# Optimization experiments

Hardware: AMD Instinct MI355X
Metric: run time of the kernel (lower is better)

The kernel has to match this reference:

```python
import jax, jax.numpy as jnp
import numpy as np

SCALE = 56  # output spatial resolution, HW = 3136
K = 3       # n_neighbors for top-k softmin scoring


def avg_pool3(x):
    # F.avg_pool2d(x, 3, 1, 1) with count_include_pad=True -> zero-padded sum / 9
    s = jax.lax.reduce_window(x, 0.0, jax.lax.add, (1, 1, 3, 3), (1, 1, 1, 1),
                              ((0, 0), (0, 0), (1, 1), (1, 1)))
    return s / 9.0


def resize_to(x, hw):
    # F.interpolate(mode='bilinear', align_corners=False) == jax.image half-pixel bilinear
    B, C, _, _ = x.shape
    return jax.image.resize(x, (B, C, hw, hw), method='bilinear')


def add_coords(x):
    # CoordConv AddCoords: append normalized x/y coordinate channels in [-1, 1]
    B, C, H, W = x.shape
    xx = jnp.broadcast_to(jnp.linspace(-1.0, 1.0, W, dtype=x.dtype)[None, :], (H, W))
    yy = jnp.broadcast_to(jnp.linspace(-1.0, 1.0, H, dtype=x.dtype)[:, None], (H, W))
    xxb = jnp.broadcast_to(xx[None, None], (B, 1, H, W))
    yyb = jnp.broadcast_to(yy[None, None], (B, 1, H, W))
    return jnp.concatenate([x, xxb, yyb], axis=1)


def setup_inputs() -> dict:
    key = jax.random.key(0)
    k1, k2, k3, k4, k5 = jax.random.split(key, 5)
    p1 = jax.random.normal(k1, (8, 256, 56, 56), dtype=jnp.float32)
    p2 = jax.random.normal(k2, (8, 512, 28, 28), dtype=jnp.float32)
    p3 = jax.random.normal(k3, (8, 1024, 14, 14), dtype=jnp.float32)
    W = jax.random.normal(k4, (1792, 1794), dtype=jnp.float32) * 0.02  # 1x1 CoordConv weight
    b = jnp.zeros((1792,), dtype=jnp.float32)
    C = jax.random.normal(k5, (1792, 3136), dtype=jnp.float32) * 0.05  # centroid bank
    return {"p1": p1, "p2": p2, "p3": p3, "W": W, "b": b, "C": C}


def reference(p1, p2, p3, W, b, C):
    # Descriptor: smooth each pyramid level, upsample to 56x56, concat -> (B,1792,56,56)
    o1 = avg_pool3(p1)
    o2 = resize_to(avg_pool3(p2), SCALE)
    o3 = resize_to(avg_pool3(p3), SCALE)
    sample = jnp.concatenate([o1, o2, o3], axis=1)
    # CoordConv 1x1
    xc = add_coords(sample)  # (B, 1794, 56, 56)
    phi = jnp.einsum('bchw,oc->bohw', xc, W) + b[None, :, None, None]
    B = phi.shape[0]
    phi_p = phi.reshape(B, 1792, SCALE * SCALE).transpose(0, 2, 1)  # (B, HW, C)
    # pairwise squared distances via expansion + matmul: (B, HW, 3136)
    features = jnp.sum(phi_p * phi_p, axis=2, keepdims=True)
    centers = jnp.sum(C * C, axis=0, keepdims=True)
    dist = features + centers - 2.0 * jnp.matmul(phi_p, C)
    dist = jnp.sqrt(jnp.maximum(dist, 0.0))
    # top-K smallest distances (ascending, like torch.topk(largest=False))
    vals = -jax.lax.top_k(-dist, K)[0]  # (B, HW, K)
    w = jax.nn.softmax(-vals, axis=-1)  # softmin
    score = w[..., 0] * vals[..., 0]    # (B, HW)
    score = score.reshape(B, 1, SCALE, SCALE)
    return score
```

## Files before the change

kernel.cpp:

```cpp
#include <hip/hip_runtime.h>
#include <math.h>
#include <stdint.h>

typedef float f32x4 __attribute__((ext_vector_type(4)));
typedef short short8 __attribute__((ext_vector_type(8)));

static constexpr int HWo   = 3136;
static constexpr int NB    = 8;
static constexpr int NP    = 3200;
static constexpr int KDIM  = 1794;
static constexpr int KP1   = 1856;
static constexpr int ODIM  = 1792;
static constexpr int NCENT = 3136;
static constexpr int NHB   = 50;
static constexpr int NHBV  = 49;

__device__ __forceinline__ uint16_t f2bf(float f) {
  union { float f; uint32_t u; } v; v.f = f;
  uint32_t u = v.u;
  return (uint16_t)((u + 0x7FFFu + ((u >> 16) & 1u)) >> 16);
}
__device__ __forceinline__ float bf2f(uint16_t h) {
  union { uint32_t u; float f; } v; v.u = ((uint32_t)h) << 16;
  return v.f;
}

__device__ __forceinline__ void gld16(const uint16_t* __restrict__ g, uint16_t* l) {
  __builtin_amdgcn_global_load_lds(
      (const __attribute__((address_space(1))) uint16_t*)g,
      (__attribute__((address_space(3))) uint16_t*)l,
      16, 0, 0);
}

__device__ __forceinline__ int xcd_swizzle(int bid, int nwg) {
  int q = nwg >> 3, r = nwg & 7;
  int xcd = bid & 7, idx = bid >> 3;
  int base = (xcd < r) ? xcd * (q + 1) : r * (q + 1) + (xcd - r) * q;
  return base + idx;
}

__global__ __launch_bounds__(256) void convW_kernel(const float* __restrict__ W, uint16_t* __restrict__ Wh) {
  int idx = blockIdx.x * 256 + threadIdx.x;
  int o = idx / KP1, k = idx % KP1;
  float v = (k < KDIM) ? W[(size_t)o * KDIM + k] : 0.f;
  Wh[idx] = f2bf(v);
}

__global__ __launch_bounds__(256) void convC_kernel(const float* __restrict__ C, uint16_t* __restrict__ Ct) {
  __shared__ float tile[64][65];
  int bj = blockIdx.x * 64;
  int bo = blockIdx.y * 64;
  int tx = threadIdx.x & 63, ty = threadIdx.x >> 6;
  #pragma unroll
  for (int s = 0; s < 16; ++s) {
    int o = ty + s * 4;
    tile[o][tx] = C[(size_t)(bo + o) * NCENT + bj + tx];
  }
  __syncthreads();
  #pragma unroll
  for (int s = 0; s < 16; ++s) {
    int j = ty + s * 4;
    Ct[(size_t)(bj + j) * ODIM + bo + tx] = f2bf(tile[tx][j]);
  }
}

__global__ __launch_bounds__(256) void rownorm_kernel(const uint16_t* __restrict__ src, float* __restrict__ dst) {
  int t = threadIdx.x, lane = t & 63, wave = t >> 6;
  int row = blockIdx.x * 4 + wave;
  const uint32_t* p = (const uint32_t*)(src + (size_t)row * ODIM);
  float s = 0.f;
  #pragma unroll
  for (int it = 0; it < 14; ++it) {
    uint32_t u = p[it * 64 + lane];
    float a = bf2f((uint16_t)(u & 0xFFFF)), b = bf2f((uint16_t)(u >> 16));
    s += a * a + b * b;
  }
  #pragma unroll
  for (int m = 1; m < 64; m <<= 1) s += __shfl_xor(s, m, 64);
  if (lane == 0) dst[row] = s;
}

__global__ __launch_bounds__(256) void zerof_kernel(float* __restrict__ p, int n) {
  int i = blockIdx.x * 256 + threadIdx.x;
  if (i < n) p[i] = 0.f;
}

static constexpr int P1SZ = 256 * 3136;
static constexpr int P2SZ = 512 * 784;
static constexpr int P3SZ = 1024 * 196;
static constexpr int PTOT = P1SZ + P2SZ + P3SZ;

__device__ __forceinline__ float pool9f(const float* __restrict__ p, int S, int y, int x) {
  float s = 0.f;
  for (int dy = -1; dy <= 1; ++dy) {
    int yy = y + dy; if (yy < 0 || yy >= S) continue;
    for (int dx = -1; dx <= 1; ++dx) {
      int xx = x + dx; if (xx < 0 || xx >= S) continue;
      s += p[yy * S + xx];
    }
  }
  return s * (1.f / 9.f);
}

__global__ __launch_bounds__(256) void pool_kernel(const float* __restrict__ p1, const float* __restrict__ p2,
                                                   const float* __restrict__ p3, float* __restrict__ pooled, int g0) {
  int b = g0 + blockIdx.y;
  float* pb = pooled + (size_t)blockIdx.y * PTOT;
  int idx = blockIdx.x * 256 + threadIdx.x;
  const float* src; int S, loc;
  if (idx < P1SZ)              { src = p1 + (size_t)b * P1SZ; S = 56; loc = idx; }
  else if (idx < P1SZ + P2SZ)  { src = p2 + (size_t)b * P2SZ; S = 28; loc = idx - P1SZ; }
  else                         { src = p3 + (size_t)b * P3SZ; S = 14; loc = idx - P1SZ - P2SZ; }
  int c = loc / (S * S), hw = loc % (S * S);
  pb[idx] = pool9f(src + (size_t)c * S * S, S, hw / S, hw % S);
}

__global__ __launch_bounds__(256) void assemble_kernel(const float* __restrict__ pooled, uint16_t* __restrict__ xcb) {
  int bg = blockIdx.y;
  const float* pb = pooled + (size_t)bg * PTOT;
  uint16_t* xb = xcb + (size_t)bg * NP * KP1;
  int idx = blockIdx.x * 256 + threadIdx.x;
  int i = idx / KP1, ch = idx % KP1;
  int x = i % 56, y = i / 56;
  float v;
  if (ch < 256) {
    v = pb[ch * 3136 + i];
  } else if (ch < 1792) {
    const float* base; int S; float scale, shift;
    if (ch < 768) { base = pb + P1SZ + (ch - 256) * 784;          S = 28; scale = 0.5f;  shift = -0.25f;  }
    else          { base = pb + P1SZ + P2SZ + (ch - 768) * 196;   S = 14; scale = 0.25f; shift = -0.375f; }
    float sx = x * scale + shift, sy = y * scale + shift;
    float fx0 = floorf(sx), fy0 = floorf(sy);
    float fx = sx - fx0, fy = sy - fy0;
    int x0 = (int)fx0, y0 = (int)fy0, x1 = x0 + 1, y1 = y0 + 1;
    x0 = x0 < 0 ? 0 : x0; x1 = x1 > S - 1 ? S - 1 : x1;
    y0 = y0 < 0 ? 0 : y0; y1 = y1 > S - 1 ? S - 1 : y1;
    float v00 = base[y0 * S + x0], v01 = base[y0 * S + x1];
    float v10 = base[y1 * S + x0], v11 = base[y1 * S + x1];
    v = (1.f - fy) * ((1.f - fx) * v00 + fx * v01) + fy * ((1.f - fx) * v10 + fx * v11);
  } else if (ch == 1792) v = -1.f + 2.f * x / 55.f;
  else if (ch == 1793)   v = -1.f + 2.f * y / 55.f;
  else                   v = 0.f;
  xb[idx] = f2bf(v);
}

__global__ __launch_bounds__(256) void gemm1_mfma(const uint16_t* __restrict__ Wh, const float* __restrict__ bias,
                                                  const uint16_t* __restrict__ xcb, uint16_t* __restrict__ phi_t,
                                                  float* __restrict__ feat) {
  __shared__ union { uint16_t ab[2][128][64]; uint16_t tr[128][136]; } sm;
  int wid = xcd_swizzle(blockIdx.x, gridDim.x);
  int row0 = (wid % 14) * 128;
  int col0 = (wid / 14) * 128;
  int t = threadIdx.x;
  int lane = t & 63, wave = t >> 6;
  int wm = wave & 1, wn = wave >> 1;
  int l15 = lane & 15, quad = lane >> 4;
  int rr = wave * 8 + (lane >> 3);
  int sg = ((lane & 7) ^ (lane >> 3)) * 8;
  f32x4 acc[4][4] = {};
  for (int k0 = 0; k0 < KP1; k0 += 64) {
    #pragma unroll
    for (int i = 0; i < 4; ++i) {
      gld16(&Wh [(size_t)(row0 + i * 32 + rr) * KP1 + k0 + sg], &sm.ab[0][i * 32 + wave * 8][0]);
      gld16(&xcb[(size_t)(col0 + i * 32 + rr) * KP1 + k0 + sg], &sm.ab[1][i * 32 + wave * 8][0]);
    }
    __syncthreads();
    #pragma unroll
    for (int kk = 0; kk < 2; ++kk) {
      short8 a[4], b[4];
      #pragma unroll
      for (int i = 0; i < 4; ++i) {
        int r = wm * 64 + i * 16 + l15;
        a[i] = *(const short8*)&sm.ab[0][r][((quad + 4 * kk) ^ (r & 7)) * 8];
      }
      #pragma unroll
      for (int j = 0; j < 4; ++j) {
        int r = wn * 64 + j * 16 + l15;
        b[j] = *(const short8*)&sm.ab[1][r][((quad + 4 * kk) ^ (r & 7)) * 8];
      }
      #pragma unroll
      for (int i = 0; i < 4; ++i)
        #pragma unroll
        for (int j = 0; j < 4; ++j)
          acc[i][j] = __builtin_amdgcn_mfma_f32_16x16x32_bf16(a[i], b[j], acc[i][j], 0, 0, 0);
    }
    __syncthreads();
  }
  #pragma unroll
  for (int i = 0; i < 4; ++i) {
    int o4 = wm * 64 + i * 16 + quad * 4;
    float4 bv = *(const float4*)&bias[row0 + o4];
    #pragma unroll
    for (int j = 0; j < 4; ++j) {
      int p = wn * 64 + j * 16 + l15;
      ushort4 u;
      u.x = f2bf(acc[i][j][0] + bv.x);
      u.y = f2bf(acc[i][j][1] + bv.y);
      u.z = f2bf(acc[i][j][2] + bv.z);
      u.w = f2bf(acc[i][j][3] + bv.w);
      *(ushort4*)&sm.tr[p][o4] = u;
    }
  }
  __syncthreads();
  int c = t & 15, prb = t >> 4;
  #pragma unroll
  for (int s = 0; s < 8; ++s) {
    int pr = s * 16 + prb;
    uint4 v = *(const uint4*)&sm.tr[pr][c * 8];
    *(uint4*)&phi_t[(size_t)(col0 + pr) * ODIM + row0 + c * 8] = v;
    const uint16_t* pv = (const uint16_t*)&v;
    float ssq = 0.f;
    #pragma unroll
    for (int e = 0; e < 8; ++e) { float f = bf2f(pv[e]); ssq += f * f; }
    #pragma unroll
    for (int m = 1; m < 16; m <<= 1) ssq += __shfl_xor(ssq, m, 16);
    if (c == 0) atomicAdd(&feat[col0 + pr], ssq);
  }
}

__device__ __forceinline__ void ins3(float v, float& a, float& b, float& c) {
  if (v < c) {
    if (v < b) { c = b; if (v < a) { b = a; a = v; } else { b = v; } }
    else { c = v; }
  }
}

__global__ __launch_bounds__(256) void gemm2_mfma(const uint16_t* __restrict__ phi_t, const uint16_t* __restrict__ Ct,
                                                  const float* __restrict__ cent, float* __restrict__ partial) {
  __shared__ uint16_t As[128][64];
  __shared__ uint16_t Bs[128][64];
  int wid = xcd_swizzle(blockIdx.x, gridDim.x);
  int col0 = (wid % 25) * 128;
  int row0 = (wid / 25) * 128;
  int t = threadIdx.x;
  int lane = t & 63, wave = t >> 6;
  int wc = wave & 1;
  int wp = wave >> 1;
  int l15 = lane & 15, quad = lane >> 4;
  int rr = wave * 8 + (lane >> 3);
  int sg = ((lane & 7) ^ (lane >> 3)) * 8;
  f32x4 acc[4][4] = {};
  for (int k0 = 0; k0 < ODIM; k0 += 64) {
    #pragma unroll
    for (int i = 0; i < 4; ++i) {
      gld16(&phi_t[(size_t)(row0 + i * 32 + rr) * ODIM + k0 + sg], &As[i * 32 + wave * 8][0]);
      gld16(&Ct   [(size_t)(col0 + i * 32 + rr) * ODIM + k0 + sg], &Bs[i * 32 + wave * 8][0]);
    }
    __syncthreads();
    #pragma unroll
    for (int kk = 0; kk < 2; ++kk) {
      short8 ac[4], bp[4];
      #pragma unroll
      for (int i = 0; i < 4; ++i) {
        int r = wc * 64 + i * 16 + l15;
        ac[i] = *(const short8*)&Bs[r][((quad + 4 * kk) ^ (r & 7)) * 8];
      }
      #pragma unroll
      for (int j = 0; j < 4; ++j) {
        int r = wp * 64 + j * 16 + l15;
        bp[j] = *(const short8*)&As[r][((quad + 4 * kk) ^ (r & 7)) * 8];
      }
      #pragma unroll
      for (int i = 0; i < 4; ++i)
        #pragma unroll
        for (int j = 0; j < 4; ++j)
          acc[i][j] = __builtin_amdgcn_mfma_f32_16x16x32_bf16(ac[i], bp[j], acc[i][j], 0, 0, 0);
    }
    __syncthreads();
  }
  if (col0 + wc * 64 < NCENT) {
    float4 cv[4];
    #pragma unroll
    for (int i = 0; i < 4; ++i)
      cv[i] = *(const float4*)&cent[col0 + wc * 64 + i * 16 + quad * 4];
    int hb = (col0 >> 6) + wc;
    #pragma unroll
    for (int j = 0; j < 4; ++j) {
      float t0 = 3.4e38f, t1 = 3.4e38f, t2 = 3.4e38f;
      #pragma unroll
      for (int i = 0; i < 4; ++i) {
        float c4[4] = {cv[i].x, cv[i].y, cv[i].z, cv[i].w};
        #pragma unroll
        for (int r = 0; r < 4; ++r)
          ins3(c4[r] - 2.f * acc[i][j][r], t0, t1, t2);
      }
      #pragma unroll
      for (int m = 16; m < 64; m <<= 1) {
        float u0 = __shfl_xor(t0, m, 64);
        float u1 = __shfl_xor(t1, m, 64);
        float u2 = __shfl_xor(t2, m, 64);
        ins3(u0, t0, t1, t2); ins3(u1, t0, t1, t2); ins3(u2, t0, t1, t2);
      }
      if (quad == 0) {
        int pix = row0 + wp * 64 + j * 16 + l15;
        float* pp = &partial[((size_t)pix * NHB + hb) * 3];
        pp[0] = t0; pp[1] = t1; pp[2] = t2;
      }
    }
  }
}

__global__ __launch_bounds__(256) void score_kernel(const float* __restrict__ partial, const float* __restrict__ feat,
                                                    float* __restrict__ out, int g0) {
  int t = threadIdx.x, lane = t & 63, wave = t >> 6;
  int gi = blockIdx.x * 4 + wave;
  int bg = gi / HWo, row = gi - bg * HWo;
  int grow = bg * NP + row;
  float t0 = 3.4e38f, t1 = 3.4e38f, t2 = 3.4e38f;
  if (lane < NHBV) {
    const float* pp = &partial[((size_t)grow * NHB + lane) * 3];
    ins3(pp[0], t0, t1, t2); ins3(pp[1], t0, t1, t2); ins3(pp[2], t0, t1, t2);
  }
  #pragma unroll
  for (int m = 1; m < 64; m <<= 1) {
    float u0 = __shfl_xor(t0, m, 64);
    float u1 = __shfl_xor(t1, m, 64);
    float u2 = __shfl_xor(t2, m, 64);
    ins3(u0, t0, t1, t2); ins3(u1, t0, t1, t2); ins3(u2, t0, t1, t2);
  }
  if (lane == 0) {
    float ft = feat[grow];
    float v0 = sqrtf(fmaxf(ft + t0, 0.f));
    float v1 = sqrtf(fmaxf(ft + t1, 0.f));
    float v2 = sqrtf(fmaxf(ft + t2, 0.f));
    float w0 = 1.f / (1.f + expf(v0 - v1) + expf(v0 - v2));
    out[(size_t)(g0 + bg) * HWo + row] = v0 * w0;
  }
}

extern "C" void kernel_launch(void* const* d_in, const int* in_sizes, int n_in,
                              void* d_out, int out_size, void* d_ws, size_t ws_size,
                              hipStream_t stream) {
  const float* p1   = (const float*)d_in[0];
  const float* p2   = (const float*)d_in[1];
  const float* p3   = (const float*)d_in[2];
  const float* Wm   = (const float*)d_in[3];
  const float* bias = (const float*)d_in[4];
  const float* Cm   = (const float*)d_in[5];
  float* out = (float*)d_out;

  const size_t szWh   = (size_t)ODIM * KP1 * 2;
  const size_t szCt   = (size_t)NP * ODIM * 2;
  const size_t szCent = (size_t)NP * 4;
  const size_t szXcb  = (size_t)NP * KP1 * 2;
  const size_t szPhi  = (size_t)NP * ODIM * 2;
  const size_t szPart = (size_t)NP * NHB * 3 * 4;
  const size_t szFeat = (size_t)NP * 4;
  const size_t fixedSz = szWh + szCt + szCent;
  const size_t perSz   = szXcb + szPhi + szPart + szFeat;
  int GB = 8;
  while (GB > 1 && fixedSz + perSz * (size_t)GB > ws_size) GB >>= 1;

  char* ws = (char*)d_ws;
  size_t off = 0;
  uint16_t* Wh     = (uint16_t*)(ws + off); off += szWh;
  uint16_t* Ct     = (uint16_t*)(ws + off); off += szCt;
  float*    cent   = (float*)(ws + off);    off += szCent;
  uint16_t* xcb    = (uint16_t*)(ws + off); off += szXcb * GB;
  uint16_t* phi_t  = (uint16_t*)(ws + off);
  float*    pooled = (float*)(ws + off);    off += szPhi * GB;
  float*    partial= (float*)(ws + off);    off += szPart * GB;
  float*    feat   = (float*)(ws + off);    off += szFeat * GB;

  convW_kernel<<<(ODIM * KP1) / 256, 256, 0, stream>>>(Wm, Wh);
  convC_kernel<<<dim3(NCENT / 64, ODIM / 64), 256, 0, stream>>>(Cm, Ct);
  rownorm_kernel<<<784, 256, 0, stream>>>(Ct, cent);

  for (int g0 = 0; g0 < NB; g0 += GB) {
    pool_kernel<<<dim3(PTOT / 256, GB), 256, 0, stream>>>(p1, p2, p3, pooled, g0);
    assemble_kernel<<<dim3((HWo * KP1) / 256, GB), 256, 0, stream>>>(pooled, xcb);
    zerof_kernel<<<(NP * GB) / 256, 256, 0, stream>>>(feat, NP * GB);
    gemm1_mfma<<<GB * 25 * 14, 256, 0, stream>>>(Wh, bias, xcb, phi_t, feat);
    gemm2_mfma<<<GB * 25 * 25, 256, 0, stream>>>(phi_t, Ct, cent, partial);
    score_kernel<<<GB * HWo / 4, 256, 0, stream>>>(partial, feat, out, g0);
  }
}
```

Baseline: 1.239 ms.

## Retile distance GEMM to 256x256 blocks with double-buffered LDS pipeline

Rewrites the distance GEMM to use 256x256 output tiles with 512 threads and double-buffered LDS. The next k-tile's global-to-LDS loads are issued while MFMAs run, with barriers and s_setprio interleaving. The centroid bank is padded to 3328 rows with a zeroed tail, and the pixel dimension is clamped so tiles can span batch boundaries. This aims to raise operand reuse and hide load latency, at the cost of 128KB of LDS per block, high register pressure and a more intricate synchronisation scheme.

```diff
diff --git a/kernel.cpp b/kernel.cpp
--- a/kernel.cpp
+++ b/kernel.cpp
@@ -12,8 +12,8 @@
 static constexpr int KP1   = 1856;
 static constexpr int ODIM  = 1792;
 static constexpr int NCENT = 3136;
-static constexpr int NHB   = 50;
-static constexpr int NHBV  = 49;
+static constexpr int NPC   = 3328;
+static constexpr int NHB   = 49;
 
 __device__ __forceinline__ uint16_t f2bf(float f) {
   union { float f; uint32_t u; } v; v.f = f;
@@ -225,76 +225,131 @@
   }
 }
 
-__global__ __launch_bounds__(256) void gemm2_mfma(const uint16_t* __restrict__ phi_t, const uint16_t* __restrict__ Ct,
-                                                  const float* __restrict__ cent, float* __restrict__ partial) {
-  __shared__ uint16_t As[128][64];
-  __shared__ uint16_t Bs[128][64];
+#define STG_A(b, h, kofs) \
+  gld16(gAp[h][0] + (kofs), &lds[b][0][(h) * 128 + wave * 16][0]); \
+  gld16(gAp[h][1] + (kofs), &lds[b][0][(h) * 128 + wave * 16 + 8][0]);
+#define STG_B(b, h, kofs) \
+  gld16(gBp[h][0] + (kofs), &lds[b][1][(h) * 128 + wave * 16][0]); \
+  gld16(gBp[h][1] + (kofs), &lds[b][1][(h) * 128 + wave * 16 + 8][0]);
+#define LDA(buf, fi, kk) (*(const short8*)&lds[buf][0][wm * 128 + (fi) * 16 + l15][(((quad) + 4 * (kk)) ^ (l15 & 7)) * 8])
+#define LDB(buf, fj, kk) (*(const short8*)&lds[buf][1][wn * 64 + (fj) * 16 + l15][(((quad) + 4 * (kk)) ^ (l15 & 7)) * 8])
+
+__global__ __launch_bounds__(512, 2) void gemm2_mfma(const uint16_t* __restrict__ phi_t, const uint16_t* __restrict__ Ct,
+                                                     const float* __restrict__ cent, float* __restrict__ partial,
+                                                     int GBNP) {
+  __shared__ uint16_t lds[2][2][256][64];
   int wid = xcd_swizzle(blockIdx.x, gridDim.x);
-  int col0 = (wid % 25) * 128;
-  int row0 = (wid / 25) * 128;
-  int t = threadIdx.x;
-  int lane = t & 63, wave = t >> 6;
-  int wc = wave & 1;
-  int wp = wave >> 1;
+  int cb = wid % 13, pb = wid / 13;
+  int col0 = cb * 256;
+  int row0 = pb * 256;
+  int t = threadIdx.x, lane = t & 63, wave = t >> 6;
+  int wm = wave & 1, wn = wave >> 1;
   int l15 = lane & 15, quad = lane >> 4;
-  int rr = wave * 8 + (lane >> 3);
-  int sg = ((lane & 7) ^ (lane >> 3)) * 8;
-  f32x4 acc[4][4] = {};
-  for (int k0 = 0; k0 < ODIM; k0 += 64) {
-    #pragma unroll
-    for (int i = 0; i < 4; ++i) {
-      gld16(&phi_t[(size_t)(row0 + i * 32 + rr) * ODIM + k0 + sg], &As[i * 32 + wave * 8][0]);
-      gld16(&Ct   [(size_t)(col0 + i * 32 + rr) * ODIM + k0 + sg], &Bs[i * 32 + wave * 8][0]);
-    }
-    __syncthreads();
-    #pragma unroll
-    for (int kk = 0; kk < 2; ++kk) {
-      short8 ac[4], bp[4];
-      #pragma unroll
-      for (int i = 0; i < 4; ++i) {
-        int r = wc * 64 + i * 16 + l15;
-        ac[i] = *(const short8*)&Bs[r][((quad + 4 * kk) ^ (r & 7)) * 8];
-      }
-      #pragma unroll
-      for (int j = 0; j < 4; ++j) {
-        int r = wp * 64 + j * 16 + l15;
-        bp[j] = *(const short8*)&As[r][((quad + 4 * kk) ^ (r & 7)) * 8];
-      }
-      #pragma unroll
-      for (int i = 0; i < 4; ++i)
+  int srow = lane >> 3;
+  int sg = ((lane & 7) ^ srow) * 8;
+  const uint16_t* gAp[2][2];
+  const uint16_t* gBp[2][2];
+  #pragma unroll
+  for (int h = 0; h < 2; ++h)
+    #pragma unroll
+    for (int i = 0; i < 2; ++i) {
+      int ra = col0 + h * 128 + wave * 16 + i * 8 + srow;
+      int rb = row0 + h * 128 + wave * 16 + i * 8 + srow;
+      rb = rb < GBNP ? rb : GBNP - 1;
+      gAp[h][i] = Ct    + (size_t)ra * ODIM + sg;
+      gBp[h][i] = phi_t + (size_t)rb * ODIM + sg;
+    }
+  f32x4 acc[8][4] = {};
+  STG_A(0, 0, 0) STG_A(0, 1, 0) STG_B(0, 0, 0) STG_B(0, 1, 0)
+  asm volatile("s_waitcnt vmcnt(0)" ::: "memory");
+  __builtin_amdgcn_s_barrier();
+  short8 af[4], bf[4];
+  for (int kt = 0; kt < 28; ++kt) {
+    int cur = kt & 1, nxt = cur ^ 1;
+    int kn = (kt + 1) * 64;
+    bool pf = (kt + 1 < 28);
+    if (pf) { STG_A(nxt, 0, kn) STG_A(nxt, 1, kn) }
+    #pragma unroll
+    for (int fj = 0; fj < 4; ++fj) bf[fj] = LDB(cur, fj, 0);
+    #pragma unroll
+    for (int fi = 0; fi < 4; ++fi) af[fi] = LDA(cur, fi, 0);
+    __builtin_amdgcn_s_barrier();
+    __builtin_amdgcn_s_setprio(1);
+    #pragma unroll
+    for (int fi = 0; fi < 4; ++fi)
+      #pragma unroll
+      for (int fj = 0; fj < 4; ++fj)
+        acc[fi][fj] = __builtin_amdgcn_mfma_f32_16x16x32_bf16(af[fi], bf[fj], acc[fi][fj], 0, 0, 0);
+    __builtin_amdgcn_s_setprio(0);
+    __builtin_amdgcn_s_barrier();
+    if (pf) { STG_B(nxt, 0, kn) STG_B(nxt, 1, kn) }
+    #pragma unroll
+    for (int fi = 0; fi < 4; ++fi) af[fi] = LDA(cur, fi + 4, 0);
+    __builtin_amdgcn_s_barrier();
+    __builtin_amdgcn_s_setprio(1);
+    #pragma unroll
+    for (int fi = 0; fi < 4; ++fi)
+      #pragma unroll
+      for (int fj = 0; fj < 4; ++fj)
+        acc[fi + 4][fj] = __builtin_amdgcn_mfma_f32_16x16x32_bf16(af[fi], bf[fj], acc[fi + 4][fj], 0, 0, 0);
+    __builtin_amdgcn_s_setprio(0);
+    __builtin_amdgcn_s_barrier();
+    #pragma unroll
+    for (int fj = 0; fj < 4; ++fj) bf[fj] = LDB(cur, fj, 1);
+    #pragma unroll
+    for (int fi = 0; fi < 4; ++fi) af[fi] = LDA(cur, fi, 1);
+    __builtin_amdgcn_s_barrier();
+    __builtin_amdgcn_s_setprio(1);
+    #pragma unroll
+    for (int fi = 0; fi < 4; ++fi)
+      #pragma unroll
+      for (int fj = 0; fj < 4; ++fj)
+        acc[fi][fj] = __builtin_amdgcn_mfma_f32_16x16x32_bf16(af[fi], bf[fj], acc[fi][fj], 0, 0, 0);
+    __builtin_amdgcn_s_setprio(0);
+    __builtin_amdgcn_s_barrier();
+    #pragma unroll
+    for (int fi = 0; fi < 4; ++fi) af[fi] = LDA(cur, fi + 4, 1);
+    __builtin_amdgcn_s_barrier();
+    __builtin_amdgcn_s_setprio(1);
+    #pragma unroll
+    for (int fi = 0; fi < 4; ++fi)
+      #pragma unroll
+      for (int fj = 0; fj < 4; ++fj)
+        acc[fi + 4][fj] = __builtin_amdgcn_mfma_f32_16x16x32_bf16(af[fi], bf[fj], acc[fi + 4][fj], 0, 0, 0);
+    __builtin_amdgcn_s_setprio(0);
+    if (pf) asm volatile("s_waitcnt vmcnt(0)" ::: "memory");
+    __builtin_amdgcn_s_barrier();
+  }
+  #pragma unroll
+  for (int hbl = 0; hbl < 2; ++hbl) {
+    if (col0 + wm * 128 + hbl * 64 < NCENT) {
+      int hb = (col0 >> 6) + wm * 2 + hbl;
+      float4 cv[4];
+      #pragma unroll
+      for (int f = 0; f < 4; ++f)
+        cv[f] = *(const float4*)&cent[col0 + wm * 128 + (hbl * 4 + f) * 16 + quad * 4];
+      #pragma unroll
+      for (int fj = 0; fj < 4; ++fj) {
+        float t0 = 3.4e38f, t1 = 3.4e38f, t2 = 3.4e38f;
         #pragma unroll
-        for (int j = 0; j < 4; ++j)
-          acc[i][j] = __builtin_amdgcn_mfma_f32_16x16x32_bf16(ac[i], bp[j], acc[i][j], 0, 0, 0);
-    }
-    __syncthreads();
-  }
-  if (col0 + wc * 64 < NCENT) {
-    float4 cv[4];
-    #pragma unroll
-    for (int i = 0; i < 4; ++i)
-      cv[i] = *(const float4*)&cent[col0 + wc * 64 + i * 16 + quad * 4];
-    int hb = (col0 >> 6) + wc;
-    #pragma unroll
-    for (int j = 0; j < 4; ++j) {
-      float t0 = 3.4e38f, t1 = 3.4e38f, t2 = 3.4e38f;
-      #pragma unroll
-      for (int i = 0; i < 4; ++i) {
-        float c4[4] = {cv[i].x, cv[i].y, cv[i].z, cv[i].w};
+        for (int f = 0; f < 4; ++f) {
+          float c4[4] = {cv[f].x, cv[f].y, cv[f].z, cv[f].w};
+          #pragma unroll
+          for (int r = 0; r < 4; ++r)
+            ins3(c4[r] - 2.f * acc[hbl * 4 + f][fj][r], t0, t1, t2);
+        }
         #pragma unroll
-        for (int r = 0; r < 4; ++r)
-          ins3(c4[r] - 2.f * acc[i][j][r], t0, t1, t2);
-      }
-      #pragma unroll
-      for (int m = 16; m < 64; m <<= 1) {
-        float u0 = __shfl_xor(t0, m, 64);
-        float u1 = __shfl_xor(t1, m, 64);
-        float u2 = __shfl_xor(t2, m, 64);
-        ins3(u0, t0, t1, t2); ins3(u1, t0, t1, t2); ins3(u2, t0, t1, t2);
-      }
-      if (quad == 0) {
-        int pix = row0 + wp * 64 + j * 16 + l15;
-        float* pp = &partial[((size_t)pix * NHB + hb) * 3];
-        pp[0] = t0; pp[1] = t1; pp[2] = t2;
+        for (int m = 16; m < 64; m <<= 1) {
+          float u0 = __shfl_xor(t0, m, 64);
+          float u1 = __shfl_xor(t1, m, 64);
+          float u2 = __shfl_xor(t2, m, 64);
+          ins3(u0, t0, t1, t2); ins3(u1, t0, t1, t2); ins3(u2, t0, t1, t2);
+        }
+        int pix = row0 + wn * 64 + fj * 16 + l15;
+        if (quad == 0 && pix < GBNP) {
+          float* pp = &partial[((size_t)pix * NHB + hb) * 3];
+          pp[0] = t0; pp[1] = t1; pp[2] = t2;
+        }
       }
     }
   }
@@ -307,7 +362,7 @@
   int bg = gi / HWo, row = gi - bg * HWo;
   int grow = bg * NP + row;
   float t0 = 3.4e38f, t1 = 3.4e38f, t2 = 3.4e38f;
-  if (lane < NHBV) {
+  if (lane < NHB) {
     const float* pp = &partial[((size_t)grow * NHB + lane) * 3];
     ins3(pp[0], t0, t1, t2); ins3(pp[1], t0, t1, t2); ins3(pp[2], t0, t1, t2);
   }
@@ -340,8 +395,8 @@
   float* out = (float*)d_out;
 
   const size_t szWh   = (size_t)ODIM * KP1 * 2;
-  const size_t szCt   = (size_t)NP * ODIM * 2;
-  const size_t szCent = (size_t)NP * 4;
+  const size_t szCt   = (size_t)NPC * ODIM * 2;
+  const size_t szCent = (size_t)NPC * 4;
   const size_t szXcb  = (size_t)NP * KP1 * 2;
   const size_t szPhi  = (size_t)NP * ODIM * 2;
   const size_t szPart = (size_t)NP * NHB * 3 * 4;
@@ -364,14 +419,17 @@
 
   convW_kernel<<<(ODIM * KP1) / 256, 256, 0, stream>>>(Wm, Wh);
   convC_kernel<<<dim3(NCENT / 64, ODIM / 64), 256, 0, stream>>>(Cm, Ct);
-  rownorm_kernel<<<784, 256, 0, stream>>>(Ct, cent);
+  zerof_kernel<<<672, 256, 0, stream>>>((float*)(Ct + (size_t)NCENT * ODIM), 172032);
+  rownorm_kernel<<<NPC / 4, 256, 0, stream>>>(Ct, cent);
 
   for (int g0 = 0; g0 < NB; g0 += GB) {
+    int GBNP = GB * NP;
+    int npb = (GBNP + 255) / 256;
     pool_kernel<<<dim3(PTOT / 256, GB), 256, 0, stream>>>(p1, p2, p3, pooled, g0);
     assemble_kernel<<<dim3((HWo * KP1) / 256, GB), 256, 0, stream>>>(pooled, xcb);
     zerof_kernel<<<(NP * GB) / 256, 256, 0, stream>>>(feat, NP * GB);
     gemm1_mfma<<<GB * 25 * 14, 256, 0, stream>>>(Wh, bias, xcb, phi_t, feat);
-    gemm2_mfma<<<GB * 25 * 25, 256, 0, stream>>>(phi_t, Ct, cent, partial);
+    gemm2_mfma<<<13 * npb, 512, 0, stream>>>(phi_t, Ct, cent, partial, GBNP);
     score_kernel<<<GB * HWo / 4, 256, 0, stream>>>(partial, feat, out, g0);
   }
 }
```

Measured after the change: 1.291 ms. 4.2% more time.

## Split assemble into transposed level-1 copy, row-staged bilinear upsample, coord fill

Applied to the files above, without the earlier changes.

The single gather-based assemble kernel becomes three kernels. The level-1 channels are transposed through a shared-memory tile so both the reads and the bf16 writes are coalesced. The level-2/3 bilinear upsample stages the two needed source rows per output row in shared memory and writes channel-contiguous output. Coordinate and padding channels are written by a small separate kernel. This targets the uncoalesced strided reads of the old per-element gather, at the cost of two extra kernel launches per batch group.

```diff
diff --git a/kernel.cpp b/kernel.cpp
--- a/kernel.cpp
+++ b/kernel.cpp
@@ -115,33 +115,80 @@
   pb[idx] = pool9f(src + (size_t)c * S * S, S, hw / S, hw % S);
 }
 
-__global__ __launch_bounds__(256) void assemble_kernel(const float* __restrict__ pooled, uint16_t* __restrict__ xcb) {
-  int bg = blockIdx.y;
+__global__ __launch_bounds__(256) void asmA_kernel(const float* __restrict__ pooled, uint16_t* __restrict__ xcb) {
+  __shared__ float tile[64][65];
+  int bg = blockIdx.z;
   const float* pb = pooled + (size_t)bg * PTOT;
   uint16_t* xb = xcb + (size_t)bg * NP * KP1;
+  int p0 = blockIdx.x * 64;
+  int c0 = blockIdx.y * 64;
+  int tx = threadIdx.x & 63, ty = threadIdx.x >> 6;
+  #pragma unroll
+  for (int s = 0; s < 16; ++s) {
+    int c = ty + s * 4;
+    tile[c][tx] = pb[(size_t)(c0 + c) * HWo + p0 + tx];
+  }
+  __syncthreads();
+  #pragma unroll
+  for (int s = 0; s < 16; ++s) {
+    int p = ty + s * 4;
+    xb[(size_t)(p0 + p) * KP1 + c0 + tx] = f2bf(tile[tx][p]);
+  }
+}
+
+__global__ __launch_bounds__(256) void asmB_kernel(const float* __restrict__ pooled, uint16_t* __restrict__ xcb) {
+  __shared__ float rows[2][128][29];
+  int bg = blockIdx.z;
+  const float* pb = pooled + (size_t)bg * PTOT;
+  uint16_t* xb = xcb + (size_t)bg * NP * KP1;
+  int y = blockIdx.x;
+  int ct = blockIdx.y;
+  bool lvl2 = ct < 4;
+  int S = lvl2 ? 28 : 14;
+  float scale = lvl2 ? 0.5f : 0.25f;
+  float shift = lvl2 ? -0.25f : -0.375f;
+  int chbase = lvl2 ? 256 + ct * 128 : 768 + (ct - 4) * 128;
+  const float* base = lvl2 ? pb + P1SZ + (size_t)(ct * 128) * 784
+                           : pb + P1SZ + P2SZ + (size_t)((ct - 4) * 128) * 196;
+  int planesz = S * S;
+  float sy = y * scale + shift;
+  float fy0 = floorf(sy);
+  float fy = sy - fy0;
+  int y0 = (int)fy0, y1 = y0 + 1;
+  y0 = y0 < 0 ? 0 : y0; y1 = y1 > S - 1 ? S - 1 : y1;
+  int t = threadIdx.x;
+  int tot = 128 * 2 * S;
+  for (int idx = t; idx < tot; idx += 256) {
+    int r = idx / S, e = idx - r * S;
+    int c = r >> 1, yr = r & 1;
+    rows[yr][c][e] = base[(size_t)c * planesz + (yr ? y1 : y0) * S + e];
+  }
+  __syncthreads();
+  int c = t & 127, xs = t >> 7;
+  #pragma unroll
+  for (int xi = 0; xi < 28; ++xi) {
+    int x = xi * 2 + xs;
+    float sx = x * scale + shift;
+    float fx0 = floorf(sx);
+    float fx = sx - fx0;
+    int x0 = (int)fx0, x1 = x0 + 1;
+    x0 = x0 < 0 ? 0 : x0; x1 = x1 > S - 1 ? S - 1 : x1;
+    float v00 = rows[0][c][x0], v01 = rows[0][c][x1];
+    float v10 = rows[1][c][x0], v11 = rows[1][c][x1];
+    float v = (1.f - fy) * ((1.f - fx) * v00 + fx * v01) + fy * ((1.f - fx) * v10 + fx * v11);
+    xb[(size_t)(y * 56 + x) * KP1 + chbase + c] = f2bf(v);
+  }
+}
+
+__global__ __launch_bounds__(256) void asmC_kernel(uint16_t* __restrict__ xcb) {
+  int bg = blockIdx.y;
+  uint16_t* xb = xcb + (size_t)bg * NP * KP1;
   int idx = blockIdx.x * 256 + threadIdx.x;
-  int i = idx / KP1, ch = idx % KP1;
+  int i = idx >> 6, ch = 1792 + (idx & 63);
   int x = i % 56, y = i / 56;
-  float v;
-  if (ch < 256) {
-    v = pb[ch * 3136 + i];
-  } else if (ch < 1792) {
-    const float* base; int S; float scale, shift;
-    if (ch < 768) { base = pb + P1SZ + (ch - 256) * 784;          S = 28; scale = 0.5f;  shift = -0.25f;  }
-    else          { base = pb + P1SZ + P2SZ + (ch - 768) * 196;   S = 14; scale = 0.25f; shift = -0.375f; }
-    float sx = x * scale + shift, sy = y * scale + shift;
-    float fx0 = floorf(sx), fy0 = floorf(sy);
-    float fx = sx - fx0, fy = sy - fy0;
-    int x0 = (int)fx0, y0 = (int)fy0, x1 = x0 + 1, y1 = y0 + 1;
-    x0 = x0 < 0 ? 0 : x0; x1 = x1 > S - 1 ? S - 1 : x1;
-    y0 = y0 < 0 ? 0 : y0; y1 = y1 > S - 1 ? S - 1 : y1;
-    float v00 = base[y0 * S + x0], v01 = base[y0 * S + x1];
-    float v10 = base[y1 * S + x0], v11 = base[y1 * S + x1];
-    v = (1.f - fy) * ((1.f - fx) * v00 + fx * v01) + fy * ((1.f - fx) * v10 + fx * v11);
-  } else if (ch == 1792) v = -1.f + 2.f * x / 55.f;
-  else if (ch == 1793)   v = -1.f + 2.f * y / 55.f;
-  else                   v = 0.f;
-  xb[idx] = f2bf(v);
+  float v = (ch == 1792) ? (-1.f + 2.f * x / 55.f)
+          : (ch == 1793) ? (-1.f + 2.f * y / 55.f) : 0.f;
+  xb[(size_t)i * KP1 + ch] = f2bf(v);
 }
 
 __global__ __launch_bounds__(256) void gemm1_mfma(const uint16_t* __restrict__ Wh, const float* __restrict__ bias,
@@ -368,7 +415,9 @@
 
   for (int g0 = 0; g0 < NB; g0 += GB) {
     pool_kernel<<<dim3(PTOT / 256, GB), 256, 0, stream>>>(p1, p2, p3, pooled, g0);
-    assemble_kernel<<<dim3((HWo * KP1) / 256, GB), 256, 0, stream>>>(pooled, xcb);
+    asmA_kernel<<<dim3(HWo / 64, 4, GB), 256, 0, stream>>>(pooled, xcb);
+    asmB_kernel<<<dim3(56, 12, GB), 256, 0, stream>>>(pooled, xcb);
+    asmC_kernel<<<dim3((HWo * 64) / 256, GB), 256, 0, stream>>>(xcb);
     zerof_kernel<<<(NP * GB) / 256, 256, 0, stream>>>(feat, NP * GB);
     gemm1_mfma<<<GB * 25 * 14, 256, 0, stream>>>(Wh, bias, xcb, phi_t, feat);
     gemm2_mfma<<<GB * 25 * 25, 256, 0, stream>>>(phi_t, Ct, cent, partial);
```

Result: faster. 993.4 us (-19.8%).
